# Optimization experiments

Hardware: AMD Instinct MI355X
Metric: run time of the kernel (lower is better)

The kernel has to match this reference:

```python
import jax, jax.numpy as jnp
import numpy as np

N_USERS = 6144
N_ITEMS = 12288
N_NODES = N_USERS + N_ITEMS
D = 64
AVG_DEG = 32
NNZ = N_NODES * AVG_DEG
N_LAYERS = 2
K = 30  # module keeps top (k+1) per row


def setup_inputs() -> dict:
    key = jax.random.key(0)
    k1, k2, k3, k4, k5 = jax.random.split(key, 5)
    user_emb = 0.1 * jax.random.normal(k1, (N_USERS, D), dtype=jnp.float32)
    item_emb = 0.1 * jax.random.normal(k2, (N_ITEMS, D), dtype=jnp.float32)
    edge_row = jax.random.randint(k3, (NNZ,), 0, N_NODES, dtype=jnp.int32)
    edge_col = jax.random.randint(k4, (NNZ,), 0, N_NODES, dtype=jnp.int32)
    # normalized-adjacency-like values (positive, ~1/deg scale)
    edge_val = jax.random.uniform(k5, (NNZ,), dtype=jnp.float32) / AVG_DEG
    return {
        "user_emb": user_emb,
        "item_emb": item_emb,
        "edge_row": edge_row,
        "edge_col": edge_col,
        "edge_val": edge_val,
    }


def _spmm(edge_row, edge_col, edge_val, x):
    # y[r] = sum_{(r,c) in E} val * x[c]   -- torch.sparse.mm equivalent (COO)
    return jax.ops.segment_sum(edge_val[:, None] * x[edge_col], edge_row,
                               num_segments=N_NODES)


def reference(user_emb, item_emb, edge_row, edge_col, edge_val):
    # LightGCN propagation
    all_emb = jnp.concatenate([user_emb, item_emb], axis=0)  # [N, D]
    embs = [all_emb]
    for _ in range(N_LAYERS):
        all_emb = _spmm(edge_row, edge_col, edge_val, all_emb)
        embs.append(all_emb)
    light_out = jnp.mean(jnp.stack(embs, axis=1), axis=1)  # [N, D]

    items = light_out[N_USERS:]  # [N_ITEMS, D]
    # F.normalize(dim=1, p=2) with eps clamp
    norm = jnp.linalg.norm(items, axis=1, keepdims=True)
    items = items / jnp.maximum(norm, 1e-12)

    # dense pairwise similarity
    sim = items @ items.T  # [N_ITEMS, N_ITEMS]

    # top_k: keep top (k+1) values per row, zero elsewhere
    vals, idx = jax.lax.top_k(sim, K + 1)  # [N_ITEMS, K+1]
    rows = jnp.arange(sim.shape[0])[:, None]
    sparse_sim = jnp.zeros_like(sim).at[rows, idx].set(vals)

    # apply_non_linearity('relu', i) -> relu
    return jax.nn.relu(sparse_sim)
```

## Files before the change

kernel.cpp:

```cpp
#include <hip/hip_runtime.h>
#include <hip/hip_bf16.h>

#define N_USERS 6144
#define N_ITEMS 12288
#define N_NODES 18432
#define D 64
#define NNZ 589824
#define K_TOP 31
#define NCAND_MIN 96
#define CMAX 256

using frag_ab = __attribute__((ext_vector_type(8))) short;
using frag_cd = __attribute__((ext_vector_type(4))) float;
using uint4_e = __attribute__((ext_vector_type(4))) unsigned;
using uint2_e = __attribute__((ext_vector_type(2))) unsigned;
using float4_e = __attribute__((ext_vector_type(4))) float;

__device__ inline unsigned f32_to_bf16_bits(float f) {
    unsigned b = __float_as_uint(f);
    return (b + 0x7FFFu + ((b >> 16) & 1u)) >> 16;
}
__device__ inline unsigned char sim_to_u8(float v) {
    float e = rintf(fmaf(v, 127.5f, 127.5f));
    e = fminf(fmaxf(e, 0.f), 255.f);
    return (unsigned char)(int)e;
}

__global__ void concat64_kernel(const float* __restrict__ u,
                                const float* __restrict__ it,
                                double* __restrict__ e0) {
    int i = blockIdx.x * 256 + threadIdx.x;
    const int NU = N_USERS * D;
    e0[i] = (i < NU) ? (double)u[i] : (double)it[i - NU];
}

__global__ void count_kernel(const int* __restrict__ er, int* __restrict__ cnt) {
    int e = blockIdx.x * 256 + threadIdx.x;
    atomicAdd(&cnt[er[e]], 1);
}

__global__ __launch_bounds__(256) void scanA_kernel(const int* __restrict__ cnt,
                                                    int* __restrict__ excl,
                                                    int* __restrict__ bsum) {
    __shared__ int sh[256];
    int t = threadIdx.x, b = blockIdx.x;
    int idx = b * 256 + t;
    int v = cnt[idx];
    sh[t] = v;
    __syncthreads();
    for (int off = 1; off < 256; off <<= 1) {
        int x = sh[t];
        int y = (t >= off) ? sh[t - off] : 0;
        __syncthreads();
        sh[t] = x + y;
        __syncthreads();
    }
    excl[idx] = sh[t] - v;
    if (t == 255) bsum[b] = sh[255];
}

__global__ __launch_bounds__(128) void scanB_kernel(const int* __restrict__ bsum,
                                                    int* __restrict__ bpre) {
    __shared__ int sh[128];
    int t = threadIdx.x;
    const int NB = N_NODES / 256;
    int v = (t < NB) ? bsum[t] : 0;
    sh[t] = v;
    __syncthreads();
    for (int off = 1; off < 128; off <<= 1) {
        int x = sh[t];
        int y = (t >= off) ? sh[t - off] : 0;
        __syncthreads();
        sh[t] = x + y;
        __syncthreads();
    }
    if (t < NB) bpre[t] = sh[t] - v;
}

__global__ __launch_bounds__(256) void scanC_kernel(const int* __restrict__ excl,
                                                    const int* __restrict__ bpre,
                                                    int* __restrict__ row_start,
                                                    int* __restrict__ cursor) {
    int idx = blockIdx.x * 256 + threadIdx.x;
    int v = excl[idx] + bpre[idx >> 8];
    row_start[idx] = v;
    cursor[idx] = v;
    if (idx == 0) row_start[N_NODES] = NNZ;
}

__global__ void scatter_kernel(const int* __restrict__ er, const int* __restrict__ ec,
                               const float* __restrict__ ev,
                               int* __restrict__ cursor, int2* __restrict__ ep) {
    int e = blockIdx.x * 256 + threadIdx.x;
    int r = er[e];
    int pos = atomicAdd(&cursor[r], 1);
    ep[pos] = make_int2(ec[e], __float_as_int(ev[e]));
}

__global__ __launch_bounds__(256) void spmm_csr_kernel(const int* __restrict__ row_start,
                                                       const int2* __restrict__ ep,
                                                       const double* __restrict__ x,
                                                       double* __restrict__ y) {
    int t = threadIdx.x;
    int lane = t & 63, wave = t >> 6;
    int row = blockIdx.x * 4 + wave;
    if (row >= N_NODES) return;
    int beg = row_start[row], end = row_start[row + 1];
    double a0 = 0.0, a1 = 0.0, a2 = 0.0, a3 = 0.0;
    int j = beg;
    int n4 = beg + ((end - beg) & ~3);
    for (; j < n4; j += 4) {
        int2 p0 = ep[j], p1 = ep[j + 1], p2 = ep[j + 2], p3 = ep[j + 3];
        a0 += (double)__int_as_float(p0.y) * x[(size_t)p0.x * D + lane];
        a1 += (double)__int_as_float(p1.y) * x[(size_t)p1.x * D + lane];
        a2 += (double)__int_as_float(p2.y) * x[(size_t)p2.x * D + lane];
        a3 += (double)__int_as_float(p3.y) * x[(size_t)p3.x * D + lane];
    }
    for (; j < end; ++j) {
        int2 p = ep[j];
        a0 += (double)__int_as_float(p.y) * x[(size_t)p.x * D + lane];
    }
    y[(size_t)row * D + lane] = (a0 + a1) + (a2 + a3);
}

__global__ void mean_norm64_kernel(const double* __restrict__ e0,
                                   const double* __restrict__ e1,
                                   const double* __restrict__ e2,
                                   double* __restrict__ xn64,
                                   ushort* __restrict__ xh) {
    int t = threadIdx.x;
    int wave = t >> 6, lane = t & 63;
    int r = blockIdx.x * 4 + wave;
    size_t g = (size_t)(r + N_USERS) * D + lane;
    double s = (e0[g] + e1[g] + e2[g]) / 3.0;
    double ss = s * s;
    #pragma unroll
    for (int off = 32; off; off >>= 1) ss += __shfl_xor(ss, off);
    double norm = sqrt(ss);
    double denom = fmax(norm, 1e-12);
    double v = s / denom;
    xn64[(size_t)r * D + lane] = v;
    xh[(size_t)r * D + lane] = (ushort)f32_to_bf16_bits((float)v);
}

#define LDS_STRIDE 72
#define OST_STRIDE 136
__global__ __launch_bounds__(256) void simgemm_kernel(const ushort* __restrict__ Xh,
                                                      unsigned char* __restrict__ Cu8) {
    __shared__ __align__(16) ushort S[2 * 128 * LDS_STRIDE];
    ushort* Als = S;
    ushort* Bls = S + 128 * LDS_STRIDE;
    int t = threadIdx.x;
    int bi = blockIdx.y, bj = blockIdx.x;

    #pragma unroll
    for (int p = 0; p < 4; ++p) {
        int u4 = t + 256 * p;
        int row = u4 >> 3;
        int seg = u4 & 7;
        *(uint4_e*)&Als[row * LDS_STRIDE + seg * 8] =
            *(const uint4_e*)&Xh[(size_t)(bi * 128 + row) * D + seg * 8];
        *(uint4_e*)&Bls[row * LDS_STRIDE + seg * 8] =
            *(const uint4_e*)&Xh[(size_t)(bj * 128 + row) * D + seg * 8];
    }
    __syncthreads();

    int lane = t & 63, wave = t >> 6;
    int wrow = (wave >> 1) * 64, wcol = (wave & 1) * 64;
    int ml = lane & 15, quad = lane >> 4;

    frag_cd acc[4][4] = {};
    #pragma unroll
    for (int s = 0; s < 2; ++s) {
        frag_ab af[4], bf[4];
        int koff = s * 32 + quad * 8;
        #pragma unroll
        for (int rt = 0; rt < 4; ++rt)
            af[rt] = *(const frag_ab*)&Als[(wrow + rt * 16 + ml) * LDS_STRIDE + koff];
        #pragma unroll
        for (int ct = 0; ct < 4; ++ct)
            bf[ct] = *(const frag_ab*)&Bls[(wcol + ct * 16 + ml) * LDS_STRIDE + koff];
        #pragma unroll
        for (int rt = 0; rt < 4; ++rt)
            #pragma unroll
            for (int ct = 0; ct < 4; ++ct)
                acc[rt][ct] = __builtin_amdgcn_mfma_f32_16x16x32_bf16(
                    af[rt], bf[ct], acc[rt][ct], 0, 0, 0);
    }
    __syncthreads();

    unsigned char* Ost = (unsigned char*)S;
    #pragma unroll
    for (int rt = 0; rt < 4; ++rt) {
        #pragma unroll
        for (int ct = 0; ct < 4; ++ct) {
            int row = wrow + rt * 16 + quad * 4;
            int col = wcol + ct * 16 + ml;
            #pragma unroll
            for (int r = 0; r < 4; ++r)
                Ost[(row + r) * OST_STRIDE + col] = sim_to_u8(acc[rt][ct][r]);
        }
    }
    __syncthreads();

    const size_t base = (size_t)(bi * 128) * N_ITEMS + bj * 128;
    #pragma unroll
    for (int p = 0; p < 8; ++p) {
        int i = t + 256 * p;
        int row = i >> 4, seg = i & 15;
        uint2_e v = *(const uint2_e*)&Ost[row * OST_STRIDE + seg * 8];
        __builtin_nontemporal_store(v, (uint2_e*)(Cu8 + base + (size_t)row * N_ITEMS + seg * 8));
    }
}

__global__ __launch_bounds__(256) void topk_kernel(const unsigned char* __restrict__ Cu8,
                                                   float* __restrict__ Cout,
                                                   const double* __restrict__ xn64) {
    __shared__ int s_red[4];
    __shared__ unsigned s_cnt;
    __shared__ int    candi[CMAX];
    __shared__ double candv[CMAX];
    __shared__ double s_xr[D];
    int t = threadIdx.x;
    int r = blockIdx.x;
    const uint4_e* Crow4 = (const uint4_e*)(Cu8 + (size_t)r * N_ITEMS);

    unsigned char u[48];
    #pragma unroll
    for (int j = 0; j < 3; ++j) {
        uint4_e f = __builtin_nontemporal_load(&Crow4[t + 256 * j]);
        #pragma unroll
        for (int q = 0; q < 4; ++q) {
            unsigned w = f[q];
            u[j * 16 + q * 4 + 0] = (unsigned char)(w & 0xFF);
            u[j * 16 + q * 4 + 1] = (unsigned char)((w >> 8) & 0xFF);
            u[j * 16 + q * 4 + 2] = (unsigned char)((w >> 16) & 0xFF);
            u[j * 16 + q * 4 + 3] = (unsigned char)(w >> 24);
        }
    }
    if (t < D) s_xr[t] = xn64[(size_t)r * D + t];

    int lo = 0, hi = 255;
    #pragma unroll
    for (int it = 0; it < 8; ++it) {
        int mid = (lo + hi + 1) >> 1;
        int c = 0;
        #pragma unroll
        for (int k = 0; k < 48; ++k) c += ((int)u[k] >= mid) ? 1 : 0;
        #pragma unroll
        for (int off = 32; off; off >>= 1) c += __shfl_down(c, off);
        if ((t & 63) == 0) s_red[t >> 6] = c;
        __syncthreads();
        int ctot = s_red[0] + s_red[1] + s_red[2] + s_red[3];
        __syncthreads();
        if (ctot >= NCAND_MIN) lo = mid; else hi = mid - 1;
    }
    int T = lo;

    if (t == 0) s_cnt = 0;
    __syncthreads();
    #pragma unroll
    for (int k = 0; k < 48; ++k) {
        if ((int)u[k] >= T) {
            unsigned pos = atomicAdd(&s_cnt, 1u);
            if (pos < CMAX) candi[pos] = 16 * (t + 256 * (k >> 4)) + (k & 15);
        }
    }
    __syncthreads();
    int c = (int)s_cnt; if (c > CMAX) c = CMAX;

    if (t < c) {
        const double* xc = xn64 + (size_t)candi[t] * D;
        double acc = 0.0;
        #pragma unroll 8
        for (int k = 0; k < D; ++k) acc += s_xr[k] * xc[k];
        candv[t] = acc;
    }
    __syncthreads();

    int   sel_idx = -1;
    float sel_val = 0.f;
    if (t < c) {
        double v = candv[t];
        int    id = candi[t];
        int rank = 0;
        for (int j = 0; j < c; ++j) {
            double vj = candv[j];
            rank += (vj > v || (vj == v && candi[j] < id)) ? 1 : 0;
        }
        if (rank < K_TOP) {
            sel_idx = id;
            sel_val = (v > 0.0) ? (float)v : 0.f;
        }
    }

    float4_e* Orow4 = (float4_e*)(Cout + (size_t)r * N_ITEMS);
    float4_e z = {0.f, 0.f, 0.f, 0.f};
    #pragma unroll
    for (int j = 0; j < 12; ++j)
        __builtin_nontemporal_store(z, &Orow4[t + 256 * j]);
    __syncthreads();
    if (sel_idx >= 0) Cout[(size_t)r * N_ITEMS + sel_idx] = sel_val;
}

extern "C" void kernel_launch(void* const* d_in, const int* in_sizes, int n_in,
                              void* d_out, int out_size, void* d_ws, size_t ws_size,
                              hipStream_t stream) {
    const float* user_emb = (const float*)d_in[0];
    const float* item_emb = (const float*)d_in[1];
    const int*   edge_row = (const int*)d_in[2];
    const int*   edge_col = (const int*)d_in[3];
    const float* edge_val = (const float*)d_in[4];
    float* C = (float*)d_out;

    double* e0d  = (double*)d_ws;
    double* e1d  = e0d + (size_t)N_NODES * D;
    double* e2d  = e1d + (size_t)N_NODES * D;
    double* xn64 = e2d + (size_t)N_NODES * D;
    int2*   ep   = (int2*)(xn64 + (size_t)N_ITEMS * D);
    ushort* xh   = (ushort*)(ep + NNZ);
    unsigned char* Cu8 = (unsigned char*)(xh + (size_t)N_ITEMS * D);
    int*  cnt       = (int*)(Cu8 + (size_t)N_ITEMS * N_ITEMS);
    int*  excl      = cnt + N_NODES;
    int*  row_start = excl + N_NODES;
    int*  cursor    = row_start + N_NODES + 1;
    int*  bsum      = cursor + N_NODES;
    int*  bpre      = bsum + 128;

    (void)hipMemsetAsync(cnt, 0, N_NODES * sizeof(int), stream);

    concat64_kernel<<<N_NODES * D / 256, 256, 0, stream>>>(user_emb, item_emb, e0d);

    count_kernel<<<NNZ / 256, 256, 0, stream>>>(edge_row, cnt);
    scanA_kernel<<<N_NODES / 256, 256, 0, stream>>>(cnt, excl, bsum);
    scanB_kernel<<<1, 128, 0, stream>>>(bsum, bpre);
    scanC_kernel<<<N_NODES / 256, 256, 0, stream>>>(excl, bpre, row_start, cursor);
    scatter_kernel<<<NNZ / 256, 256, 0, stream>>>(edge_row, edge_col, edge_val, cursor, ep);

    spmm_csr_kernel<<<(N_NODES + 3) / 4, 256, 0, stream>>>(row_start, ep, e0d, e1d);
    spmm_csr_kernel<<<(N_NODES + 3) / 4, 256, 0, stream>>>(row_start, ep, e1d, e2d);

    mean_norm64_kernel<<<N_ITEMS / 4, 256, 0, stream>>>(e0d, e1d, e2d, xn64, xh);

    dim3 ggrid(N_ITEMS / 128, N_ITEMS / 128);
    simgemm_kernel<<<ggrid, 256, 0, stream>>>(xh, Cu8);

    topk_kernel<<<N_ITEMS, 256, 0, stream>>>(Cu8, C, xn64);
}
```

Baseline: 922.8 us.

## Fuse second SpMM with mean/normalize and exploit symmetry in similarity GEMM

The second propagation layer is computed only for item rows and fused directly into the mean+L2-normalize step, which removes the e2 buffer and one kernel launch and skips the user rows. The similarity GEMM now computes only upper-triangular tiles and writes each off-diagonal tile twice, once transposed through a second LDS staging area. This roughly halves the MFMA work and input loads, in exchange for extra LDS transpose writes and bank conflicts from the column-wise stores.

```diff
diff --git a/kernel.cpp b/kernel.cpp
--- a/kernel.cpp
+++ b/kernel.cpp
@@ -123,24 +123,43 @@
     y[(size_t)row * D + lane] = (a0 + a1) + (a2 + a3);
 }
 
-__global__ void mean_norm64_kernel(const double* __restrict__ e0,
-                                   const double* __restrict__ e1,
-                                   const double* __restrict__ e2,
-                                   double* __restrict__ xn64,
-                                   ushort* __restrict__ xh) {
-    int t = threadIdx.x;
-    int wave = t >> 6, lane = t & 63;
-    int r = blockIdx.x * 4 + wave;
-    size_t g = (size_t)(r + N_USERS) * D + lane;
-    double s = (e0[g] + e1[g] + e2[g]) / 3.0;
+__global__ __launch_bounds__(256) void spmm_norm_kernel(const int* __restrict__ row_start,
+                                                        const int2* __restrict__ ep,
+                                                        const double* __restrict__ e0,
+                                                        const double* __restrict__ e1,
+                                                        double* __restrict__ xn64,
+                                                        ushort* __restrict__ xh) {
+    int t = threadIdx.x;
+    int lane = t & 63, wave = t >> 6;
+    int ir = blockIdx.x * 4 + wave;
+    int row = ir + N_USERS;
+    int beg = row_start[row], end = row_start[row + 1];
+    double a0 = 0.0, a1 = 0.0, a2 = 0.0, a3 = 0.0;
+    int j = beg;
+    int n4 = beg + ((end - beg) & ~3);
+    for (; j < n4; j += 4) {
+        int2 p0 = ep[j], p1 = ep[j + 1], p2 = ep[j + 2], p3 = ep[j + 3];
+        a0 += (double)__int_as_float(p0.y) * e1[(size_t)p0.x * D + lane];
+        a1 += (double)__int_as_float(p1.y) * e1[(size_t)p1.x * D + lane];
+        a2 += (double)__int_as_float(p2.y) * e1[(size_t)p2.x * D + lane];
+        a3 += (double)__int_as_float(p3.y) * e1[(size_t)p3.x * D + lane];
+    }
+    for (; j < end; ++j) {
+        int2 p = ep[j];
+        a0 += (double)__int_as_float(p.y) * e1[(size_t)p.x * D + lane];
+    }
+    double e2v = (a0 + a1) + (a2 + a3);
+
+    size_t g = (size_t)row * D + lane;
+    double s = (e0[g] + e1[g] + e2v) / 3.0;
     double ss = s * s;
     #pragma unroll
     for (int off = 32; off; off >>= 1) ss += __shfl_xor(ss, off);
     double norm = sqrt(ss);
     double denom = fmax(norm, 1e-12);
     double v = s / denom;
-    xn64[(size_t)r * D + lane] = v;
-    xh[(size_t)r * D + lane] = (ushort)f32_to_bf16_bits((float)v);
+    xn64[(size_t)ir * D + lane] = v;
+    xh[(size_t)ir * D + lane] = (ushort)f32_to_bf16_bits((float)v);
 }
 
 #define LDS_STRIDE 72
@@ -148,10 +167,11 @@
 __global__ __launch_bounds__(256) void simgemm_kernel(const ushort* __restrict__ Xh,
                                                       unsigned char* __restrict__ Cu8) {
     __shared__ __align__(16) ushort S[2 * 128 * LDS_STRIDE];
+    int bi = blockIdx.y, bj = blockIdx.x;
+    if (bj < bi) return;
     ushort* Als = S;
     ushort* Bls = S + 128 * LDS_STRIDE;
     int t = threadIdx.x;
-    int bi = blockIdx.y, bj = blockIdx.x;
 
     #pragma unroll
     for (int p = 0; p < 4; ++p) {
@@ -189,7 +209,9 @@
     }
     __syncthreads();
 
-    unsigned char* Ost = (unsigned char*)S;
+    unsigned char* Ost  = (unsigned char*)S;
+    unsigned char* Ost2 = (unsigned char*)S + 128 * OST_STRIDE;
+    int offdiag = (bi != bj);
     #pragma unroll
     for (int rt = 0; rt < 4; ++rt) {
         #pragma unroll
@@ -197,19 +219,32 @@
             int row = wrow + rt * 16 + quad * 4;
             int col = wcol + ct * 16 + ml;
             #pragma unroll
-            for (int r = 0; r < 4; ++r)
-                Ost[(row + r) * OST_STRIDE + col] = sim_to_u8(acc[rt][ct][r]);
-        }
-    }
-    __syncthreads();
-
-    const size_t base = (size_t)(bi * 128) * N_ITEMS + bj * 128;
+            for (int r = 0; r < 4; ++r) {
+                unsigned char q8 = sim_to_u8(acc[rt][ct][r]);
+                Ost[(row + r) * OST_STRIDE + col] = q8;
+                if (offdiag) Ost2[col * OST_STRIDE + row + r] = q8;
+            }
+        }
+    }
+    __syncthreads();
+
+    const size_t base1 = (size_t)(bi * 128) * N_ITEMS + bj * 128;
     #pragma unroll
     for (int p = 0; p < 8; ++p) {
         int i = t + 256 * p;
         int row = i >> 4, seg = i & 15;
         uint2_e v = *(const uint2_e*)&Ost[row * OST_STRIDE + seg * 8];
-        __builtin_nontemporal_store(v, (uint2_e*)(Cu8 + base + (size_t)row * N_ITEMS + seg * 8));
+        __builtin_nontemporal_store(v, (uint2_e*)(Cu8 + base1 + (size_t)row * N_ITEMS + seg * 8));
+    }
+    if (offdiag) {
+        const size_t base2 = (size_t)(bj * 128) * N_ITEMS + bi * 128;
+        #pragma unroll
+        for (int p = 0; p < 8; ++p) {
+            int i = t + 256 * p;
+            int row = i >> 4, seg = i & 15;
+            uint2_e v = *(const uint2_e*)&Ost2[row * OST_STRIDE + seg * 8];
+            __builtin_nontemporal_store(v, (uint2_e*)(Cu8 + base2 + (size_t)row * N_ITEMS + seg * 8));
+        }
     }
 }
 
@@ -315,8 +350,7 @@
 
     double* e0d  = (double*)d_ws;
     double* e1d  = e0d + (size_t)N_NODES * D;
-    double* e2d  = e1d + (size_t)N_NODES * D;
-    double* xn64 = e2d + (size_t)N_NODES * D;
+    double* xn64 = e1d + (size_t)N_NODES * D;
     int2*   ep   = (int2*)(xn64 + (size_t)N_ITEMS * D);
     ushort* xh   = (ushort*)(ep + NNZ);
     unsigned char* Cu8 = (unsigned char*)(xh + (size_t)N_ITEMS * D);
@@ -337,10 +371,8 @@
     scanC_kernel<<<N_NODES / 256, 256, 0, stream>>>(excl, bpre, row_start, cursor);
     scatter_kernel<<<NNZ / 256, 256, 0, stream>>>(edge_row, edge_col, edge_val, cursor, ep);
 
-    spmm_csr_kernel<<<(N_NODES + 3) / 4, 256, 0, stream>>>(row_start, ep, e0d, e1d);
-    spmm_csr_kernel<<<(N_NODES + 3) / 4, 256, 0, stream>>>(row_start, ep, e1d, e2d);
-
-    mean_norm64_kernel<<<N_ITEMS / 4, 256, 0, stream>>>(e0d, e1d, e2d, xn64, xh);
+    spmm_csr_kernel<<<N_NODES / 4, 256, 0, stream>>>(row_start, ep, e0d, e1d);
+    spmm_norm_kernel<<<N_ITEMS / 4, 256, 0, stream>>>(row_start, ep, e0d, e1d, xn64, xh);
 
     dim3 ggrid(N_ITEMS / 128, N_ITEMS / 128);
     simgemm_kernel<<<ggrid, 256, 0, stream>>>(xh, Cu8);
```

New measurement: 908.5 us. No clear change (-1.5%).
